# Kernel optimization log

Measured on AMD Instinct MI355X. Metric: run time of the kernel, lower is better.

## Reference

```python
import jax, jax.numpy as jnp
import numpy as np

B, CIN, COUT, H, W = 4, 256, 256, 64, 64


def setup_inputs() -> dict:
    key = jax.random.key(0)
    ks = jax.random.split(key, 7)
    x = jax.random.normal(ks[0], (B, CIN, H, W), dtype=jnp.float32)
    s = 1.0 / np.sqrt(CIN)
    Wq = jax.random.uniform(ks[1], (COUT, CIN), jnp.float32, -s, s)
    Wk = jax.random.uniform(ks[2], (COUT, CIN), jnp.float32, -s, s)
    Wv = jax.random.uniform(ks[3], (COUT, CIN), jnp.float32, -s, s)
    bq = jax.random.uniform(ks[4], (COUT,), jnp.float32, -s, s)
    bk = jax.random.uniform(ks[5], (COUT,), jnp.float32, -s, s)
    bv = jax.random.uniform(ks[6], (COUT,), jnp.float32, -s, s)
    return {"x": x, "Wq": Wq, "Wk": Wk, "Wv": Wv, "bq": bq, "bk": bk, "bv": bv}


def reference(x, Wq, Wk, Wv, bq, bk, bv):
    b, cin, h, w = x.shape
    xf = x.reshape(b, cin, h * w)  # [B, Cin, N]
    # 1x1 conv == channel matmul
    q = jnp.einsum('oc,bcn->bon', Wq, xf) + bq[None, :, None]  # [B, C, N]
    k = jnp.einsum('oc,bcn->bon', Wk, xf) + bk[None, :, None]
    v = jnp.einsum('oc,bcn->bon', Wv, xf) + bv[None, :, None]
    # attention over flattened spatial positions (no 1/sqrt(d) scaling, as in source)
    scores = jnp.einsum('bcn,bcm->bnm', q, k)          # [B, N, N]
    attn = jax.nn.softmax(scores, axis=-1)
    out = jnp.einsum('bnm,bcm->bcn', attn, v)          # [B, C, N]
    return out.reshape(b, q.shape[1], h, w)
```

## Files before the change

### kernel.cpp

```cpp
#include <hip/hip_runtime.h>


typedef _Float16 f16;
typedef f16 f16x4 __attribute__((ext_vector_type(4)));
typedef f16 f16x8 __attribute__((ext_vector_type(8)));
typedef float f32x16 __attribute__((ext_vector_type(16)));

#define NB 4
#define NC 256
#define NN 4096
#define KVSPLIT 4
#define KRANGE (NN / KVSPLIT)
#define NCHUNK (KRANGE / 64)

typedef const __attribute__((address_space(1))) void* gas_t;
typedef __attribute__((address_space(3))) void* las_t;

__device__ __forceinline__ void load_lds16(const void* g, void* l) {
    __builtin_amdgcn_global_load_lds((gas_t)g, (las_t)l, 16, 0, 0);
}

__global__ __launch_bounds__(256) void wcvt_kernel(
    const float* __restrict__ Wq, const float* __restrict__ Wk,
    const float* __restrict__ Wv, f16* __restrict__ Wh)
{
    const int idx = blockIdx.x * 256 + threadIdx.x;
    const float* s = (idx < 65536) ? Wq : (idx < 131072 ? Wk : Wv);
    Wh[idx] = (f16)s[idx & 65535];
}

__global__ __launch_bounds__(256) void qkv_mfma_kernel(
    const float* __restrict__ x, const f16* __restrict__ Wh,
    const float* __restrict__ bq, const float* __restrict__ bk, const float* __restrict__ bv,
    f16* __restrict__ Qh, f16* __restrict__ Kh, f16* __restrict__ Vt)
{
    const int b  = blockIdx.y;
    const int n0 = blockIdx.x * 64;
    const int t  = threadIdx.x;
    const int wv = t >> 6, l = t & 63, ln = l & 31, g = l >> 5;

    __shared__ char xs[64 * 512];
    __shared__ char st[32768];

    {
        const int ci0 = t >> 4;
        const int nq  = (t & 15) * 4;
        for (int it = 0; it < 16; ++it) {
            const int ci = it * 16 + ci0;
            float v4[4];
            *(float4*)v4 = *(const float4*)(x + ((size_t)b * NC + ci) * NN + n0 + nq);
            const int gr = ci >> 3, lo = (ci & 7) * 2;
            #pragma unroll
            for (int j = 0; j < 4; ++j) {
                const int n = nq + j;
                *(f16*)(xs + n * 512 + ((gr ^ (n & 7)) * 16 + lo)) = (f16)v4[j];
            }
        }
    }
    __syncthreads();

    const int c0 = wv * 64;
    for (int m = 0; m < 3; ++m) {
        const f16*  W    = Wh + m * (NC * NC);
        const float* bias = (m == 0) ? bq : (m == 1 ? bk : bv);

        f32x16 acc[2][2];
        #pragma unroll
        for (int i = 0; i < 2; ++i)
            #pragma unroll
            for (int j = 0; j < 2; ++j)
                #pragma unroll
                for (int r = 0; r < 16; ++r) acc[i][j][r] = 0.0f;

        #pragma unroll
        for (int cs = 0; cs < 16; ++cs) {
            f16x8 a0 = *(const f16x8*)(W + (size_t)(c0 + ln) * NC + cs * 16 + 8 * g);
            f16x8 a1 = *(const f16x8*)(W + (size_t)(c0 + 32 + ln) * NC + cs * 16 + 8 * g);
            const int xb = (cs * 32 + g * 16) ^ ((ln & 7) << 4);
            f16x8 b0 = *(const f16x8*)(xs + ln * 512 + xb);
            f16x8 b1 = *(const f16x8*)(xs + (32 + ln) * 512 + xb);
            acc[0][0] = __builtin_amdgcn_mfma_f32_32x32x16_f16(a0, b0, acc[0][0], 0, 0, 0);
            acc[0][1] = __builtin_amdgcn_mfma_f32_32x32x16_f16(a0, b1, acc[0][1], 0, 0, 0);
            acc[1][0] = __builtin_amdgcn_mfma_f32_32x32x16_f16(a1, b0, acc[1][0], 0, 0, 0);
            acc[1][1] = __builtin_amdgcn_mfma_f32_32x32x16_f16(a1, b1, acc[1][1], 0, 0, 0);
        }

        __syncthreads();
        if (m < 2) {
            #pragma unroll
            for (int ct = 0; ct < 2; ++ct)
                #pragma unroll
                for (int nt = 0; nt < 2; ++nt)
                    #pragma unroll
                    for (int q = 0; q < 4; ++q) {
                        const int cb = c0 + ct * 32 + 8 * q + 4 * g;
                        f16x4 pk;
                        #pragma unroll
                        for (int j = 0; j < 4; ++j)
                            pk[j] = (f16)(acc[ct][nt][q * 4 + j] + bias[cb + j]);
                        const int n  = nt * 32 + ln;
                        const int g8 = cb >> 3;
                        *(f16x4*)(st + n * 512 + ((g8 ^ (n & 7)) * 16 + (cb & 7) * 2)) = pk;
                    }
            __syncthreads();
            f16* dst = (m == 0) ? Qh : Kh;
            const int gi  = t & 31;
            const int nb8 = (t >> 5) * 8;
            #pragma unroll
            for (int k = 0; k < 8; ++k) {
                const int n = nb8 + k;
                const uint4 d = *(const uint4*)(st + n * 512 + ((gi ^ (n & 7)) << 4));
                *(uint4*)(dst + ((size_t)b * NN + n0 + n) * NC + gi * 8) = d;
            }
        } else {
            #pragma unroll
            for (int ct = 0; ct < 2; ++ct)
                #pragma unroll
                for (int nt = 0; nt < 2; ++nt) {
                    const int n  = nt * 32 + ln;
                    const int pn = (n & ~15) | (n & 3) | ((n & 8) >> 1) | ((n & 4) << 1);
                    #pragma unroll
                    for (int r = 0; r < 16; ++r) {
                        const int c = c0 + ct * 32 + (r & 3) + 8 * (r >> 2) + 4 * g;
                        *(f16*)(st + c * 128 + ((pn * 2) ^ ((c & 7) << 4))) =
                            (f16)(acc[ct][nt][r] + bias[c]);
                    }
                }
            __syncthreads();
            #pragma unroll
            for (int ci = 0; ci < 8; ++ci) {
                const int c = ci * 32 + (t >> 3);
                const int s = t & 7;
                const uint4 d = *(const uint4*)(st + c * 128 + ((s ^ (c & 7)) << 4));
                *(uint4*)(Vt + ((size_t)b * NC + c) * NN + n0 + s * 8) = d;
            }
        }
    }
}

__global__ __launch_bounds__(512, 2) void flash_mfma_kernel(
    const f16* __restrict__ Qh, const f16* __restrict__ Kh, const f16* __restrict__ Vt,
    f16* __restrict__ Op, float* __restrict__ Mst, float* __restrict__ Lst)
{
    const int t  = threadIdx.x;
    const int wv = t >> 6;
    const int l  = t & 63;
    const int ln = l & 31;
    const int g  = l >> 5;

    const int flat  = blockIdx.x;
    const int xcd   = flat & 7;
    const int slot  = flat >> 3;
    const int bs    = xcd * 2 + (slot & 1);
    const int qt    = slot >> 1;
    const int b     = bs >> 2;
    const int split = bs & 3;
    const int qrow  = qt * 256 + wv * 32 + ln;

    __shared__ char ldsK[2 * 32768];
    __shared__ char ldsV[2 * 32768];

    f16x8 qf[16];
    {
        const f16* Qb = Qh + ((size_t)b * NN + qrow) * NC;
        #pragma unroll
        for (int cs = 0; cs < 16; ++cs)
            qf[cs] = *(const f16x8*)(Qb + cs * 16 + 8 * g);
    }

    f32x16 o[8];
    #pragma unroll
    for (int ct = 0; ct < 8; ++ct)
        #pragma unroll
        for (int r = 0; r < 16; ++r) o[ct][r] = 0.0f;

    float mrun = -1e30f, lrun = 0.0f;
    const int key_base = split * KRANGE;
    const f16* KhB = Kh + (size_t)b * NN * NC;
    const f16* VtB = Vt + (size_t)b * NC * NN;

#define DMA(CH, BUF) do {                                                            \
        const int key0_ = key_base + (CH) * 64;                                      \
        _Pragma("unroll")                                                            \
        for (int j = 0; j < 4; ++j) {                                                \
            const int r2  = wv * 4 + j;                                              \
            const int row = r2 * 2 + (l >> 5);                                       \
            const int u   = (l & 31) ^ (row & 7);                                    \
            load_lds16(KhB + (size_t)(key0_ + row) * NC + u * 8,                     \
                       ldsK + (BUF) * 32768 + r2 * 1024);                            \
        }                                                                            \
        _Pragma("unroll")                                                            \
        for (int j = 0; j < 4; ++j) {                                                \
            const int c8 = wv * 4 + j;                                               \
            const int c  = c8 * 8 + (l >> 3);                                        \
            const int u  = (l & 7) ^ (c & 7);                                        \
            load_lds16(VtB + (size_t)c * NN + key0_ + u * 8,                         \
                       ldsV + (BUF) * 32768 + c8 * 1024);                            \
        }                                                                            \
    } while (0)

    DMA(0, 0);

    for (int ch = 0; ch < NCHUNK; ++ch) {
        const int cb = ch & 1;
        if (ch + 1 < NCHUNK) {
            DMA(ch + 1, cb ^ 1);
            asm volatile("s_waitcnt vmcnt(8)" ::: "memory");
        } else {
            asm volatile("s_waitcnt vmcnt(0)" ::: "memory");
        }
        __builtin_amdgcn_s_barrier();

        const char* K0 = ldsK + cb * 32768;
        const char* V0 = ldsV + cb * 32768;

        f32x16 s0, s1;
        #pragma unroll
        for (int r = 0; r < 16; ++r) { s0[r] = 0.0f; s1[r] = 0.0f; }
        const int ksw = (ln & 7) << 4;
        __builtin_amdgcn_s_setprio(1);
        #pragma unroll
        for (int cs = 0; cs < 16; ++cs) {
            const int col = (cs * 32 + g * 16) ^ ksw;
            f16x8 a0 = *(const f16x8*)(K0 + ln * 512 + col);
            f16x8 a1 = *(const f16x8*)(K0 + (32 + ln) * 512 + col);
            s0 = __builtin_amdgcn_mfma_f32_32x32x16_f16(a0, qf[cs], s0, 0, 0, 0);
            s1 = __builtin_amdgcn_mfma_f32_32x32x16_f16(a1, qf[cs], s1, 0, 0, 0);
        }
        __builtin_amdgcn_s_setprio(0);

        float mt = fmaxf(s0[0], s1[0]);
        #pragma unroll
        for (int r = 1; r < 16; ++r) mt = fmaxf(mt, fmaxf(s0[r], s1[r]));
        mt = fmaxf(mt, __shfl_xor(mt, 32));
        if (!__all(mt <= mrun + 8.0f)) {
            const float mnew  = fmaxf(mrun, mt);
            const float alpha = __expf(mrun - mnew);
            #pragma unroll
            for (int ct = 0; ct < 8; ++ct)
                #pragma unroll
                for (int r = 0; r < 16; ++r) o[ct][r] *= alpha;
            lrun *= alpha;
            mrun  = mnew;
        }

        float ps = 0.0f;
        f16x8 pf[4];
        #pragma unroll
        for (int r = 0; r < 16; ++r) {
            const float e0 = __expf(s0[r] - mrun);
            const float e1 = __expf(s1[r] - mrun);
            ps += e0 + e1;
            pf[r >> 3][r & 7]       = (f16)e0;
            pf[2 + (r >> 3)][r & 7] = (f16)e1;
        }
        ps += __shfl_xor(ps, 32);
        lrun += ps;

        const int vsw = (ln & 7) << 4;
        __builtin_amdgcn_s_setprio(1);
        #pragma unroll
        for (int ct = 0; ct < 8; ++ct) {
            const int vrow = (ct * 32 + ln) * 128;
            #pragma unroll
            for (int s = 0; s < 4; ++s) {
                f16x8 va = *(const f16x8*)(V0 + vrow + ((s * 32 + g * 16) ^ vsw));
                o[ct] = __builtin_amdgcn_mfma_f32_32x32x16_f16(va, pf[s], o[ct], 0, 0, 0);
            }
        }
        __builtin_amdgcn_s_setprio(0);

        __builtin_amdgcn_s_barrier();
    }
#undef DMA

    const float invl = 1.0f / lrun;
    #pragma unroll
    for (int ct = 0; ct < 8; ++ct)
        #pragma unroll
        for (int r = 0; r < 16; ++r) {
            const int c = ct * 32 + (r & 3) + 8 * (r >> 2) + 4 * g;
            Op[((size_t)(split * NB + b) * NC + c) * NN + qrow] = (f16)(o[ct][r] * invl);
        }
    if (g == 0) {
        Mst[(split * NB + b) * NN + qrow] = mrun;
        Lst[(split * NB + b) * NN + qrow] = lrun;
    }
}

__global__ __launch_bounds__(256) void combine_kernel(
    const f16* __restrict__ Op, const float* __restrict__ Mst, const float* __restrict__ Lst,
    float* __restrict__ out)
{
    const int t = threadIdx.x;
    const int b = blockIdx.y;
    const int n = blockIdx.x * 64 + (t & 63);

    float w[KVSPLIT];
    float mm = -1e30f;
    #pragma unroll
    for (int s = 0; s < KVSPLIT; ++s) {
        w[s] = Mst[(s * NB + b) * NN + n];
        mm = fmaxf(mm, w[s]);
    }
    float tot = 0.0f;
    #pragma unroll
    for (int s = 0; s < KVSPLIT; ++s) {
        w[s] = __expf(w[s] - mm) * Lst[(s * NB + b) * NN + n];
        tot += w[s];
    }
    const float inv = 1.0f / tot;
    #pragma unroll
    for (int s = 0; s < KVSPLIT; ++s) w[s] *= inv;

    for (int c = (t >> 6); c < NC; c += 4) {
        float acc = 0.0f;
        #pragma unroll
        for (int s = 0; s < KVSPLIT; ++s)
            acc += w[s] * (float)Op[((size_t)(s * NB + b) * NC + c) * NN + n];
        out[((size_t)b * NC + c) * NN + n] = acc;
    }
}

extern "C" void kernel_launch(void* const* d_in, const int* in_sizes, int n_in,
                              void* d_out, int out_size, void* d_ws, size_t ws_size,
                              hipStream_t stream)
{
    const float* x  = (const float*)d_in[0];
    const float* Wq = (const float*)d_in[1];
    const float* Wk = (const float*)d_in[2];
    const float* Wv = (const float*)d_in[3];
    const float* bq = (const float*)d_in[4];
    const float* bk = (const float*)d_in[5];
    const float* bv = (const float*)d_in[6];
    float* out = (float*)d_out;

    f16* Qh = (f16*)d_ws;
    f16* Kh = Qh + (size_t)NB * NN * NC;
    f16* Vt = Kh + (size_t)NB * NN * NC;
    f16* Op = Vt + (size_t)NB * NN * NC;
    float* Mst = (float*)(Op + (size_t)KVSPLIT * NB * NC * NN);
    float* Lst = Mst + (size_t)KVSPLIT * NB * NN;
    f16*  Wh  = (f16*)(Lst + (size_t)KVSPLIT * NB * NN);

    wcvt_kernel<<<768, 256, 0, stream>>>(Wq, Wk, Wv, Wh);
    qkv_mfma_kernel<<<dim3(NN / 64, NB), 256, 0, stream>>>(
        x, Wh, bq, bk, bv, Qh, Kh, Vt);
    flash_mfma_kernel<<<256, 512, 0, stream>>>(Qh, Kh, Vt, Op, Mst, Lst);
    combine_kernel<<<dim3(NN / 64, NB), 256, 0, stream>>>(Op, Mst, Lst, out);
}
```

Baseline: 131.9 us.

## Halve flash attention tile sizes: 128-query blocks of 4 waves, 32-key chunks

The flash kernel now runs 512 blocks of 256 threads, each covering 128 query rows. Keys are streamed in chunks of 32 instead of 64, which halves LDS usage per block and changes the K and V swizzle layouts to fit the smaller tiles. The goal is more blocks for scheduling and a smaller LDS footprint per CU. In exchange there are twice as many barriers and DMA rounds per key range, and each K/V tile is reused by fewer waves, so global and L2 traffic for K/V goes up.

```diff
diff --git a/kernel.cpp b/kernel.cpp
--- a/kernel.cpp
+++ b/kernel.cpp
@@ -11,7 +11,7 @@
 #define NN 4096
 #define KVSPLIT 4
 #define KRANGE (NN / KVSPLIT)
-#define NCHUNK (KRANGE / 64)
+#define NCHUNK (KRANGE / 32)
 
 typedef const __attribute__((address_space(1))) void* gas_t;
 typedef __attribute__((address_space(3))) void* las_t;
@@ -138,7 +138,7 @@
     }
 }
 
-__global__ __launch_bounds__(512, 2) void flash_mfma_kernel(
+__global__ __launch_bounds__(256, 2) void flash_mfma_kernel(
     const f16* __restrict__ Qh, const f16* __restrict__ Kh, const f16* __restrict__ Vt,
     f16* __restrict__ Op, float* __restrict__ Mst, float* __restrict__ Lst)
 {
@@ -150,15 +150,15 @@
 
     const int flat  = blockIdx.x;
     const int xcd   = flat & 7;
-    const int slot  = flat >> 3;
-    const int bs    = xcd * 2 + (slot & 1);
-    const int qt    = slot >> 1;
+    const int idx   = flat >> 3;
+    const int bs    = xcd * 2 + (idx & 1);
+    const int qt    = idx >> 1;
     const int b     = bs >> 2;
     const int split = bs & 3;
-    const int qrow  = qt * 256 + wv * 32 + ln;
-
-    __shared__ char ldsK[2 * 32768];
-    __shared__ char ldsV[2 * 32768];
+    const int qrow  = qt * 128 + wv * 32 + ln;
+
+    __shared__ char ldsK[2 * 16384];
+    __shared__ char ldsV[2 * 16384];
 
     f16x8 qf[16];
     {
@@ -180,22 +180,23 @@
     const f16* VtB = Vt + (size_t)b * NC * NN;
 
 #define DMA(CH, BUF) do {                                                            \
-        const int key0_ = key_base + (CH) * 64;                                      \
+        const int key0_ = key_base + (CH) * 32;                                      \
         _Pragma("unroll")                                                            \
         for (int j = 0; j < 4; ++j) {                                                \
             const int r2  = wv * 4 + j;                                              \
             const int row = r2 * 2 + (l >> 5);                                       \
-            const int u   = (l & 31) ^ (row & 7);                                    \
+            const int u   = (l & 31) ^ (row & 15);                                   \
             load_lds16(KhB + (size_t)(key0_ + row) * NC + u * 8,                     \
-                       ldsK + (BUF) * 32768 + r2 * 1024);                            \
+                       ldsK + (BUF) * 16384 + r2 * 1024);                            \
         }                                                                            \
         _Pragma("unroll")                                                            \
         for (int j = 0; j < 4; ++j) {                                                \
-            const int c8 = wv * 4 + j;                                               \
-            const int c  = c8 * 8 + (l >> 3);                                        \
-            const int u  = (l & 7) ^ (c & 7);                                        \
-            load_lds16(VtB + (size_t)c * NN + key0_ + u * 8,                         \
-                       ldsV + (BUF) * 32768 + c8 * 1024);                            \
+            const int i  = wv * 4 + j;                                               \
+            const int R  = i * 4 + (l >> 4);                                         \
+            const int c  = R * 4 + ((l & 15) >> 2);                                  \
+            const int kg = (l & 3) ^ (R & 3);                                        \
+            load_lds16(VtB + (size_t)c * NN + key0_ + kg * 8,                        \
+                       ldsV + (BUF) * 16384 + i * 1024);                             \
         }                                                                            \
     } while (0)
 
@@ -211,27 +212,24 @@
         }
         __builtin_amdgcn_s_barrier();
 
-        const char* K0 = ldsK + cb * 32768;
-        const char* V0 = ldsV + cb * 32768;
-
-        f32x16 s0, s1;
-        #pragma unroll
-        for (int r = 0; r < 16; ++r) { s0[r] = 0.0f; s1[r] = 0.0f; }
-        const int ksw = (ln & 7) << 4;
+        const char* K0 = ldsK + cb * 16384;
+        const char* V0 = ldsV + cb * 16384;
+
+        f32x16 s0;
+        #pragma unroll
+        for (int r = 0; r < 16; ++r) s0[r] = 0.0f;
         __builtin_amdgcn_s_setprio(1);
         #pragma unroll
         for (int cs = 0; cs < 16; ++cs) {
-            const int col = (cs * 32 + g * 16) ^ ksw;
+            const int col = ((cs * 2 + g) ^ (ln & 15)) * 16;
             f16x8 a0 = *(const f16x8*)(K0 + ln * 512 + col);
-            f16x8 a1 = *(const f16x8*)(K0 + (32 + ln) * 512 + col);
             s0 = __builtin_amdgcn_mfma_f32_32x32x16_f16(a0, qf[cs], s0, 0, 0, 0);
-            s1 = __builtin_amdgcn_mfma_f32_32x32x16_f16(a1, qf[cs], s1, 0, 0, 0);
         }
         __builtin_amdgcn_s_setprio(0);
 
-        float mt = fmaxf(s0[0], s1[0]);
-        #pragma unroll
-        for (int r = 1; r < 16; ++r) mt = fmaxf(mt, fmaxf(s0[r], s1[r]));
+        float mt = s0[0];
+        #pragma unroll
+        for (int r = 1; r < 16; ++r) mt = fmaxf(mt, s0[r]);
         mt = fmaxf(mt, __shfl_xor(mt, 32));
         if (!__all(mt <= mrun + 8.0f)) {
             const float mnew  = fmaxf(mrun, mt);
@@ -245,26 +243,25 @@
         }
 
         float ps = 0.0f;
-        f16x8 pf[4];
+        f16x8 pf[2];
         #pragma unroll
         for (int r = 0; r < 16; ++r) {
             const float e0 = __expf(s0[r] - mrun);
-            const float e1 = __expf(s1[r] - mrun);
-            ps += e0 + e1;
-            pf[r >> 3][r & 7]       = (f16)e0;
-            pf[2 + (r >> 3)][r & 7] = (f16)e1;
+            ps += e0;
+            pf[r >> 3][r & 7] = (f16)e0;
         }
         ps += __shfl_xor(ps, 32);
         lrun += ps;
 
-        const int vsw = (ln & 7) << 4;
         __builtin_amdgcn_s_setprio(1);
         #pragma unroll
         for (int ct = 0; ct < 8; ++ct) {
-            const int vrow = (ct * 32 + ln) * 128;
-            #pragma unroll
-            for (int s = 0; s < 4; ++s) {
-                f16x8 va = *(const f16x8*)(V0 + vrow + ((s * 32 + g * 16) ^ vsw));
+            const int c    = ct * 32 + ln;
+            const int base = (c >> 2) * 256 + (c & 3) * 64;
+            const int rsw  = (c >> 2) & 3;
+            #pragma unroll
+            for (int s = 0; s < 2; ++s) {
+                f16x8 va = *(const f16x8*)(V0 + base + (((s * 2 + g) ^ rsw) * 16));
                 o[ct] = __builtin_amdgcn_mfma_f32_32x32x16_f16(va, pf[s], o[ct], 0, 0, 0);
             }
         }
@@ -346,6 +343,6 @@
     wcvt_kernel<<<768, 256, 0, stream>>>(Wq, Wk, Wv, Wh);
     qkv_mfma_kernel<<<dim3(NN / 64, NB), 256, 0, stream>>>(
         x, Wh, bq, bk, bv, Qh, Kh, Vt);
-    flash_mfma_kernel<<<256, 512, 0, stream>>>(Qh, Kh, Vt, Op, Mst, Lst);
+    flash_mfma_kernel<<<512, 256, 0, stream>>>(Qh, Kh, Vt, Op, Mst, Lst);
     combine_kernel<<<dim3(NN / 64, NB), 256, 0, stream>>>(Op, Mst, Lst, out);
 }
```

After: 136.0 us. 1.03x slower.

## Fold log2e into Q projection, use exp2, widen LDS swizzles, defer row-sum shuffle

Applied to the files above, without the earlier changes.

Q is scaled by log2(e) inside the projection epilogue, so every softmax exponential becomes a plain exp2 with no extra multiply. The per-chunk cross-half shuffle of the row sum is moved to a single shuffle after the loop. The lazy-rescale threshold is raised to 12 so the output accumulators are rescaled less often. The K and V LDS swizzles are changed to a 16-way XOR for K and a paired-row layout for V to cut bank conflicts, at the cost of more complex address arithmetic and a tighter fp16 overflow margin.

```diff
diff --git a/kernel.cpp b/kernel.cpp
--- a/kernel.cpp
+++ b/kernel.cpp
@@ -63,6 +63,7 @@
     for (int m = 0; m < 3; ++m) {
         const f16*  W    = Wh + m * (NC * NC);
         const float* bias = (m == 0) ? bq : (m == 1 ? bk : bv);
+        const float qs   = (m == 0) ? 1.44269504f : 1.0f;
 
         f32x16 acc[2][2];
         #pragma unroll
@@ -97,7 +98,7 @@
                         f16x4 pk;
                         #pragma unroll
                         for (int j = 0; j < 4; ++j)
-                            pk[j] = (f16)(acc[ct][nt][q * 4 + j] + bias[cb + j]);
+                            pk[j] = (f16)((acc[ct][nt][q * 4 + j] + bias[cb + j]) * qs);
                         const int n  = nt * 32 + ln;
                         const int g8 = cb >> 3;
                         *(f16x4*)(st + n * 512 + ((g8 ^ (n & 7)) * 16 + (cb & 7) * 2)) = pk;
@@ -183,19 +184,20 @@
         const int key0_ = key_base + (CH) * 64;                                      \
         _Pragma("unroll")                                                            \
         for (int j = 0; j < 4; ++j) {                                                \
-            const int r2  = wv * 4 + j;                                              \
-            const int row = r2 * 2 + (l >> 5);                                       \
-            const int u   = (l & 31) ^ (row & 7);                                    \
+            const int ki  = wv * 4 + j;                                              \
+            const int row = ki * 2 + (l >> 5);                                       \
+            const int u   = (l & 31) ^ (row & 15);                                   \
             load_lds16(KhB + (size_t)(key0_ + row) * NC + u * 8,                     \
-                       ldsK + (BUF) * 32768 + r2 * 1024);                            \
+                       ldsK + (BUF) * 32768 + ki * 1024);                            \
         }                                                                            \
         _Pragma("unroll")                                                            \
         for (int j = 0; j < 4; ++j) {                                                \
-            const int c8 = wv * 4 + j;                                               \
-            const int c  = c8 * 8 + (l >> 3);                                        \
-            const int u  = (l & 7) ^ (c & 7);                                        \
-            load_lds16(VtB + (size_t)c * NN + key0_ + u * 8,                         \
-                       ldsV + (BUF) * 32768 + c8 * 1024);                            \
+            const int vi = wv * 4 + j;                                               \
+            const int R  = vi * 4 + (l >> 4);                                        \
+            const int c  = R * 2 + ((l & 15) >> 3);                                  \
+            const int k8 = (l & 7) ^ (R & 7);                                        \
+            load_lds16(VtB + (size_t)c * NN + key0_ + k8 * 8,                        \
+                       ldsV + (BUF) * 32768 + vi * 1024);                            \
         }                                                                            \
     } while (0)
 
@@ -217,11 +219,11 @@
         f32x16 s0, s1;
         #pragma unroll
         for (int r = 0; r < 16; ++r) { s0[r] = 0.0f; s1[r] = 0.0f; }
-        const int ksw = (ln & 7) << 4;
+        const int ksw = (ln & 15) << 4;
         __builtin_amdgcn_s_setprio(1);
         #pragma unroll
         for (int cs = 0; cs < 16; ++cs) {
-            const int col = (cs * 32 + g * 16) ^ ksw;
+            const int col = ((cs * 2 + g) << 4) ^ ksw;
             f16x8 a0 = *(const f16x8*)(K0 + ln * 512 + col);
             f16x8 a1 = *(const f16x8*)(K0 + (32 + ln) * 512 + col);
             s0 = __builtin_amdgcn_mfma_f32_32x32x16_f16(a0, qf[cs], s0, 0, 0, 0);
@@ -233,9 +235,9 @@
         #pragma unroll
         for (int r = 1; r < 16; ++r) mt = fmaxf(mt, fmaxf(s0[r], s1[r]));
         mt = fmaxf(mt, __shfl_xor(mt, 32));
-        if (!__all(mt <= mrun + 8.0f)) {
+        if (!__all(mt <= mrun + 12.0f)) {
             const float mnew  = fmaxf(mrun, mt);
-            const float alpha = __expf(mrun - mnew);
+            const float alpha = exp2f(mrun - mnew);
             #pragma unroll
             for (int ct = 0; ct < 8; ++ct)
                 #pragma unroll
@@ -248,23 +250,24 @@
         f16x8 pf[4];
         #pragma unroll
         for (int r = 0; r < 16; ++r) {
-            const float e0 = __expf(s0[r] - mrun);
-            const float e1 = __expf(s1[r] - mrun);
+            const float e0 = exp2f(s0[r] - mrun);
+            const float e1 = exp2f(s1[r] - mrun);
             ps += e0 + e1;
             pf[r >> 3][r & 7]       = (f16)e0;
             pf[2 + (r >> 3)][r & 7] = (f16)e1;
         }
-        ps += __shfl_xor(ps, 32);
         lrun += ps;
 
-        const int vsw = (ln & 7) << 4;
         __builtin_amdgcn_s_setprio(1);
         #pragma unroll
         for (int ct = 0; ct < 8; ++ct) {
-            const int vrow = (ct * 32 + ln) * 128;
+            const int c    = ct * 32 + ln;
+            const int R    = c >> 1;
+            const int base = R * 256 + (c & 1) * 128;
+            const int rsw  = R & 7;
             #pragma unroll
             for (int s = 0; s < 4; ++s) {
-                f16x8 va = *(const f16x8*)(V0 + vrow + ((s * 32 + g * 16) ^ vsw));
+                f16x8 va = *(const f16x8*)(V0 + base + (((s * 2 + g) ^ rsw) << 4));
                 o[ct] = __builtin_amdgcn_mfma_f32_32x32x16_f16(va, pf[s], o[ct], 0, 0, 0);
             }
         }
@@ -274,6 +277,7 @@
     }
 #undef DMA
 
+    lrun += __shfl_xor(lrun, 32);
     const float invl = 1.0f / lrun;
     #pragma unroll
     for (int ct = 0; ct < 8; ++ct)
@@ -306,7 +310,7 @@
     float tot = 0.0f;
     #pragma unroll
     for (int s = 0; s < KVSPLIT; ++s) {
-        w[s] = __expf(w[s] - mm) * Lst[(s * NB + b) * NN + n];
+        w[s] = exp2f(w[s] - mm) * Lst[(s * NB + b) * NN + n];
         tot += w[s];
     }
     const float inv = 1.0f / tot;
```

Result: slower. 153.9 us (+16.6%).
